# Kernel optimization log

Measured on AMD Instinct MI355X. Metric: run time of the kernel, lower is better.

Reference implementation:

```python
import jax, jax.numpy as jnp
import numpy as np

H, F = 4, 32          # num_of_heads, num_out_features
HF = H * F            # 128
F_IN = 128
EDGE_DIM = 64
HIDDEN = 256
B = 64
MLE = 1500
N = B * MLE           # 96000
E = 600000
LN_EPS = 1e-5


def setup_inputs() -> dict:
    key = jax.random.key(0)
    ks = jax.random.split(key, 20)

    def glorot(k, shape):
        fan_in, fan_out = shape[-2], shape[-1]
        lim = np.sqrt(6.0 / (fan_in + fan_out))
        return jax.random.uniform(k, shape, jnp.float32, -lim, lim)

    inp = {
        "in_nodes_features": jax.random.normal(ks[0], (N, F_IN), jnp.float32),
        "edge_index": jax.random.randint(ks[1], (2, E), 0, N),
        "edges": jax.random.normal(ks[2], (E, EDGE_DIM), jnp.float32),
        "instructions": jax.random.normal(ks[3], (B, HIDDEN), jnp.float32),
        "batch_ids": jax.random.randint(ks[4], (E,), 0, B),
        "max_local_entity": MLE,
        # parameters (stored as [in, out]; torch Linear is x @ W.T)
        "W_proj": glorot(ks[5], (F_IN, HF)),
        "W_edge": glorot(ks[6], (EDGE_DIM, HF)),
        "W_src_ins": glorot(ks[7], (HIDDEN, HF)),
        "b_src_ins": jnp.zeros((HF,), jnp.float32),
        "W_trg_ins": glorot(ks[8], (HIDDEN, HF)),
        "b_trg_ins": jnp.zeros((HF,), jnp.float32),
        "W_edge_ins": glorot(ks[9], (HIDDEN, HF)),
        "b_edge_ins": jnp.zeros((HF,), jnp.float32),
        "a_src": glorot(ks[10], (1, H, F)),
        "a_trg": glorot(ks[11], (1, H, F)),
        "a_edge": glorot(ks[12], (1, H, F)),
        "bias": jnp.zeros((HF,), jnp.float32),
        "W_skip": glorot(ks[13], (F_IN, HF)),
        "ln_gamma": jnp.ones((2 * HF,), jnp.float32),
        "ln_beta": jnp.zeros((2 * HF,), jnp.float32),
    }
    return inp


def _segment_softmax(scores, seg_idx, num_nodes):
    # scores: [E, H]; softmax over edges sharing the same seg_idx node
    s = scores - jax.lax.stop_gradient(scores.max())  # global-max shift, as in original
    e = jnp.exp(s)
    denom = jax.ops.segment_sum(e, seg_idx, num_segments=num_nodes)  # [N, H]
    return (e / (denom[seg_idx] + 1e-16))[..., None]  # [E, H, 1]


def _branch(proj, lift_idx, agg_idx, scores_per_edge, x, W_skip, bias, num_nodes):
    att = _segment_softmax(scores_per_edge, agg_idx, num_nodes)          # [E,H,1]
    weighted = proj[lift_idx] * att                                      # [E,H,F]
    out = jax.ops.segment_sum(weighted, agg_idx, num_segments=num_nodes) # [N,H,F]
    out = out + (x @ W_skip).reshape(num_nodes, H, F)                    # skip (F != F_in path)
    out = out.reshape(num_nodes, HF) + bias                              # concat heads + bias
    return out


def reference(in_nodes_features, edge_index, edges, instructions, batch_ids,
              max_local_entity, W_proj, W_edge, W_src_ins, b_src_ins,
              W_trg_ins, b_trg_ins, W_edge_ins, b_edge_ins,
              a_src, a_trg, a_edge, bias, W_skip, ln_gamma, ln_beta):
    x = in_nodes_features                      # dropout disabled (eval / p=0)
    num_nodes = x.shape[0]
    b = instructions.shape[0]
    src_idx, trg_idx = edge_index[0], edge_index[1]

    proj = (x @ W_proj).reshape(num_nodes, H, F)           # [N,H,F]
    eproj = (edges @ W_edge).reshape(-1, H, F)             # [E,H,F]

    def bridge(Wi, bi):  # instruction -> per-node [N,H,F]
        br = instructions @ Wi + bi                        # [B,HF]
        br = jnp.broadcast_to(br[:, None, :], (b, max_local_entity, HF))
        return br.reshape(num_nodes, H, F)

    src_br = bridge(W_src_ins, b_src_ins)
    trg_br = bridge(W_trg_ins, b_trg_ins)
    edge_br = (instructions @ W_edge_ins + b_edge_ins)[batch_ids].reshape(-1, H, F)

    scores_source = (proj * a_src * src_br).sum(-1)        # [N,H]
    scores_target = (proj * a_trg * trg_br).sum(-1)        # [N,H]
    scores_edge = (eproj * a_edge * edge_br).sum(-1)       # [E,H]

    scores_per_edge = jax.nn.leaky_relu(
        scores_source[src_idx] + scores_target[trg_idx] + scores_edge,
        negative_slope=0.2)                                # [E,H]

    # direction == 'all': aggregate src->trg and trg->src
    trg_feats = _branch(proj, src_idx, trg_idx, scores_per_edge, x, W_skip, bias, num_nodes)
    src_feats = _branch(proj, trg_idx, src_idx, scores_per_edge, x, W_skip, bias, num_nodes)

    out = jnp.concatenate([src_feats, trg_feats], axis=1)  # [N, 2*HF]
    mu = out.mean(-1, keepdims=True)
    var = ((out - mu) ** 2).mean(-1, keepdims=True)
    return (out - mu) * jax.lax.rsqrt(var + LN_EPS) * ln_gamma + ln_beta
```

## Files before the change

kernel.cpp:

```cpp
#include <hip/hip_runtime.h>
#include <stdint.h>

typedef unsigned short ushortT;
typedef __attribute__((ext_vector_type(8))) short short8;
typedef __attribute__((ext_vector_type(4))) float float4_;

#define HH 4
#define FF 32
#define HFD 128
#define F_IN 128
#define EDGE_DIM 64
#define HIDDEN 256
#define BB 64
#define MLE 1500
#define NN 96000
#define EEc 600000
#define CAP 32

__device__ __forceinline__ float bf_lo(uint32_t u){ return __uint_as_float(u << 16); }
__device__ __forceinline__ float bf_hi(uint32_t u){ return __uint_as_float(u & 0xffff0000u); }
__device__ __forceinline__ uint32_t f2bf(float f){
    uint32_t u = __float_as_uint(f);
    return (u + 0x7fffu + ((u >> 16) & 1u)) >> 16;
}
__device__ __forceinline__ short8 cvt8(const float* p){
    float4_ x0 = *(const float4_*)p;
    float4_ x1 = *(const float4_*)(p + 4);
    short8 r;
    r[0]=(short)f2bf(x0[0]); r[1]=(short)f2bf(x0[1]); r[2]=(short)f2bf(x0[2]); r[3]=(short)f2bf(x0[3]);
    r[4]=(short)f2bf(x1[0]); r[5]=(short)f2bf(x1[1]); r[6]=(short)f2bf(x1[2]); r[7]=(short)f2bf(x1[3]);
    return r;
}

__global__ void k_bridge(const float* ins, const float* Wsrc, const float* bsrc,
                         const float* Wtrg, const float* btrg,
                         const float* Wedg, const float* bedg,
                         const float* a_src, const float* a_trg, const float* a_edge,
                         const float* W_edge,
                         float* csrc, float* ctrg, float* Mout)
{
    __shared__ float ins_s[HIDDEN];
    __shared__ float ce_s[HFD];
    int b = blockIdx.x, t = threadIdx.x;
    const float* ip = ins + b * HIDDEN;
    ins_s[t]       = ip[t];
    ins_s[t + 128] = ip[t + 128];
    __syncthreads();
    float as = 0.f, at = 0.f, ae = 0.f;
    for (int k = 0; k < HIDDEN; k++){
        float iv = ins_s[k];
        as += iv * Wsrc[k*HFD + t];
        at += iv * Wtrg[k*HFD + t];
        ae += iv * Wedg[k*HFD + t];
    }
    csrc[b*HFD + t] = (as + bsrc[t]) * a_src[t];
    ctrg[b*HFD + t] = (at + btrg[t]) * a_trg[t];
    ce_s[t] = (ae + bedg[t]) * a_edge[t];
    __syncthreads();
    #pragma unroll
    for (int rep = 0; rep < 2; rep++){
        int idx = t + rep * 128;
        int d = idx >> 2, h = idx & 3;
        float acc = 0.f;
        #pragma unroll
        for (int f = 0; f < FF; f++)
            acc += W_edge[d*HFD + h*FF + f] * ce_s[h*FF + f];
        Mout[b*256 + d*4 + h] = acc;
    }
}

__global__ void k_transpose(const float* Wp, const float* Wsk, ushortT* WcatT)
{
    int idx = blockIdx.x * 256 + threadIdx.x;
    int c = idx >> 7;
    int d = idx & 127;
    float v = (c < 128) ? Wp[d*128 + c] : Wsk[d*128 + (c - 128)];
    WcatT[c*128 + d] = (ushortT)f2bf(v);
}

__global__ __launch_bounds__(256) void k_gemm(const float* x, const ushortT* WcatT,
                                              const float* csrc, const float* ctrg,
                                              ushortT* proj, ushortT* skip,
                                              float* s_src, float* s_trg)
{
    int t = threadIdx.x;
    int w = t >> 6, lane = t & 63;
    int q = lane >> 4, n16 = lane & 15;
    size_t node = (size_t)blockIdx.x * 64 + w * 16 + n16;

    float4_ acc[16];
    #pragma unroll
    for (int j = 0; j < 16; j++) acc[j] = (float4_){0.f, 0.f, 0.f, 0.f};

    #pragma unroll
    for (int kk = 0; kk < 4; kk++){
        short8 bfrag = cvt8(x + node * 128 + kk*32 + q*8);
        #pragma unroll
        for (int j = 0; j < 16; j++){
            short8 afrag = *(const short8*)(WcatT + (size_t)(j*16 + n16) * 128 + kk*32 + q*8);
            acc[j] = __builtin_amdgcn_mfma_f32_16x16x32_bf16(afrag, bfrag, acc[j], 0, 0, 0);
        }
    }

    #pragma unroll
    for (int j = 0; j < 16; j++){
        uint32_t p0 = f2bf(acc[j][0]) | (f2bf(acc[j][1]) << 16);
        uint32_t p1 = f2bf(acc[j][2]) | (f2bf(acc[j][3]) << 16);
        ushortT* base = (j < 8) ? (proj + node*128 + j*16 + q*4)
                                : (skip + node*128 + (j-8)*16 + q*4);
        uint2 pv; pv.x = p0; pv.y = p1;
        *(uint2*)base = pv;
    }

    int b = (int)(node / MLE);
    const float* cs = csrc + b * HFD;
    const float* ct = ctrg + b * HFD;
    float ps[4] = {0,0,0,0}, pt[4] = {0,0,0,0};
    #pragma unroll
    for (int j = 0; j < 8; j++){
        int h = j >> 1;
        #pragma unroll
        for (int r = 0; r < 4; r++){
            int c = j*16 + q*4 + r;
            ps[h] += acc[j][r] * cs[c];
            pt[h] += acc[j][r] * ct[c];
        }
    }
    #pragma unroll
    for (int m = 16; m < 64; m <<= 1){
        #pragma unroll
        for (int hh = 0; hh < 4; hh++){
            ps[hh] += __shfl_xor(ps[hh], m, 64);
            pt[hh] += __shfl_xor(pt[hh], m, 64);
        }
    }
    float vs = (q == 0) ? ps[0] : (q == 1) ? ps[1] : (q == 2) ? ps[2] : ps[3];
    float vt = (q == 0) ? pt[0] : (q == 1) ? pt[1] : (q == 2) ? pt[2] : pt[3];
    s_src[node*4 + q] = vs;
    s_trg[node*4 + q] = vt;
}

__global__ __launch_bounds__(256) void k_edges(const int* eidx, const int* bids,
    const float* edges, const float* M, const float* s_src, const float* s_trg,
    float* ex, int* cnt_src, int* cnt_trg, uint32_t* adj_src, uint32_t* adj_trg)
{
    int e = blockIdx.x * 256 + threadIdx.x;
    if (e >= EEc) return;
    int src = eidx[e];
    int trg = eidx[EEc + e];
    int bid = bids[e];
    const float* Mb = M + bid * 256;
    const float4_* er = (const float4_*)(edges + (size_t)e * EDGE_DIM);
    float se0=0.f, se1=0.f, se2=0.f, se3=0.f;
    #pragma unroll
    for (int i = 0; i < 16; i++){
        float4_ v = er[i];
        #pragma unroll
        for (int c = 0; c < 4; c++){
            int d = i*4 + c;
            float4_ m = *(const float4_*)(Mb + d*4);
            se0 += v[c]*m[0];
            se1 += v[c]*m[1];
            se2 += v[c]*m[2];
            se3 += v[c]*m[3];
        }
    }
    float4_ ssv = *(const float4_*)(s_src + (size_t)src*4);
    float4_ stv = *(const float4_*)(s_trg + (size_t)trg*4);
    float sc0 = ssv[0] + stv[0] + se0;
    float sc1 = ssv[1] + stv[1] + se1;
    float sc2 = ssv[2] + stv[2] + se2;
    float sc3 = ssv[3] + stv[3] + se3;
    sc0 = sc0 > 0.f ? sc0 : 0.2f*sc0;
    sc1 = sc1 > 0.f ? sc1 : 0.2f*sc1;
    sc2 = sc2 > 0.f ? sc2 : 0.2f*sc2;
    sc3 = sc3 > 0.f ? sc3 : 0.2f*sc3;
    float4_ exv = {__expf(sc0), __expf(sc1), __expf(sc2), __expf(sc3)};
    *(float4_*)(ex + (size_t)e*4) = exv;

    int sl = atomicAdd(&cnt_src[src], 1);
    if (sl < CAP) adj_src[(size_t)src*CAP + sl] = (uint32_t)e;
    int sl2 = atomicAdd(&cnt_trg[trg], 1);
    if (sl2 < CAP) adj_trg[(size_t)trg*CAP + sl2] = (uint32_t)e;
}

__global__ __launch_bounds__(256) void k_agg(const ushortT* proj, const ushortT* skip,
    const float* bias, const float* ex, const int* eidx,
    const int* cnt_src, const int* cnt_trg,
    const uint32_t* adj_src, const uint32_t* adj_trg,
    const float* gamma, const float* beta, float* out)
{
    __shared__ int   sh_nbr[2][4][CAP];
    __shared__ float sh_ev [2][4][CAP*4];

    int wave = threadIdx.x >> 6, lane = threadIdx.x & 63;
    int n = blockIdx.x * 4 + wave;
    int h = lane >> 4;

    int cnt0 = cnt_src[n]; if (cnt0 > CAP) cnt0 = CAP;
    int cnt1 = cnt_trg[n]; if (cnt1 > CAP) cnt1 = CAP;

    if (lane < cnt0){
        int e = (int)adj_src[(size_t)n * CAP + lane];
        sh_nbr[0][wave][lane] = eidx[EEc + e];
        *(float4_*)&sh_ev[0][wave][lane*4] = *(const float4_*)(ex + (size_t)e*4);
    }
    if (lane < cnt1){
        int e = (int)adj_trg[(size_t)n * CAP + lane];
        sh_nbr[1][wave][lane] = eidx[e];
        *(float4_*)&sh_ev[1][wave][lane*4] = *(const float4_*)(ex + (size_t)e*4);
    }

    uint32_t sv = ((const uint32_t*)(skip + (size_t)n * 128))[lane];
    float b0 = bias[2*lane], b1 = bias[2*lane + 1];

    __syncthreads();

    float sk0 = bf_lo(sv) + b0;
    float sk1 = bf_hi(sv) + b1;

    float a0 = 0.f, a1 = 0.f, ad = 0.f;
    #pragma unroll 4
    for (int i = 0; i < cnt0; i++){
        int nbr  = sh_nbr[0][wave][i];
        float ev = sh_ev[0][wave][i*4 + h];
        uint32_t pv = ((const uint32_t*)(proj + (size_t)nbr * 128))[lane];
        a0 += ev * bf_lo(pv);
        a1 += ev * bf_hi(pv);
        ad += ev;
    }
    float inv = 1.f / (ad + 1e-16f);
    float f0 = a0 * inv + sk0;
    float f1 = a1 * inv + sk1;

    a0 = 0.f; a1 = 0.f; ad = 0.f;
    #pragma unroll 4
    for (int i = 0; i < cnt1; i++){
        int nbr  = sh_nbr[1][wave][i];
        float ev = sh_ev[1][wave][i*4 + h];
        uint32_t pv = ((const uint32_t*)(proj + (size_t)nbr * 128))[lane];
        a0 += ev * bf_lo(pv);
        a1 += ev * bf_hi(pv);
        ad += ev;
    }
    inv = 1.f / (ad + 1e-16f);
    float f2 = a0 * inv + sk0;
    float f3 = a1 * inv + sk1;

    float s  = f0 + f1 + f2 + f3;
    float sq = f0*f0 + f1*f1 + f2*f2 + f3*f3;
    #pragma unroll
    for (int m = 1; m < 64; m <<= 1){
        s  += __shfl_xor(s,  m, 64);
        sq += __shfl_xor(sq, m, 64);
    }
    float mu  = s * (1.f/256.f);
    float var = sq * (1.f/256.f) - mu*mu;
    var = var < 0.f ? 0.f : var;
    float rr = rsqrtf(var + 1e-5f);

    float o0 = (f0 - mu) * rr * gamma[2*lane]           + beta[2*lane];
    float o1 = (f1 - mu) * rr * gamma[2*lane + 1]       + beta[2*lane + 1];
    float o2 = (f2 - mu) * rr * gamma[128 + 2*lane]     + beta[128 + 2*lane];
    float o3 = (f3 - mu) * rr * gamma[128 + 2*lane + 1] + beta[128 + 2*lane + 1];

    float* orow = out + (size_t)n * 256;
    *(float2*)(orow + 2*lane)       = make_float2(o0, o1);
    *(float2*)(orow + 128 + 2*lane) = make_float2(o2, o3);
}

extern "C" void kernel_launch(void* const* d_in, const int* in_sizes, int n_in,
                              void* d_out, int out_size, void* d_ws, size_t ws_size,
                              hipStream_t stream)
{
    const float* x      = (const float*)d_in[0];
    const int*   eidx   = (const int*)d_in[1];
    const float* edges  = (const float*)d_in[2];
    const float* ins    = (const float*)d_in[3];
    const int*   bids   = (const int*)d_in[4];
    const float* Wproj  = (const float*)d_in[6];
    const float* Wedge  = (const float*)d_in[7];
    const float* Wsrc   = (const float*)d_in[8];
    const float* bsrc   = (const float*)d_in[9];
    const float* Wtrg   = (const float*)d_in[10];
    const float* btrg   = (const float*)d_in[11];
    const float* Wedgi  = (const float*)d_in[12];
    const float* bedgi  = (const float*)d_in[13];
    const float* a_src  = (const float*)d_in[14];
    const float* a_trg  = (const float*)d_in[15];
    const float* a_edge = (const float*)d_in[16];
    const float* bias   = (const float*)d_in[17];
    const float* Wskip  = (const float*)d_in[18];
    const float* gamma  = (const float*)d_in[19];
    const float* beta   = (const float*)d_in[20];

    char* ws = (char*)d_ws;
    size_t off = 0;
    ushortT* proj  = (ushortT*)(ws + off); off += (size_t)NN * 128 * 2;
    ushortT* skip  = (ushortT*)(ws + off); off += (size_t)NN * 128 * 2;
    ushortT* WcatT = (ushortT*)(ws + off); off += 256 * 128 * 2;
    float*   csrc  = (float*)(ws + off);   off += BB * HFD * 4;
    float*   ctrg  = (float*)(ws + off);   off += BB * HFD * 4;
    float*   M     = (float*)(ws + off);   off += BB * 256 * 4;
    float*   s_src = (float*)(ws + off);   off += (size_t)NN * 4 * 4;
    float*   s_trg = (float*)(ws + off);   off += (size_t)NN * 4 * 4;
    float*   ex    = (float*)(ws + off);   off += (size_t)EEc * 4 * 4;
    int*     cnt_src = (int*)(ws + off);   off += (size_t)NN * 4;
    int*     cnt_trg = (int*)(ws + off);   off += (size_t)NN * 4;
    uint32_t* adj_src = (uint32_t*)(ws + off); off += (size_t)NN * CAP * 4;
    uint32_t* adj_trg = (uint32_t*)(ws + off); off += (size_t)NN * CAP * 4;

    hipMemsetAsync(cnt_src, 0, (size_t)NN * 4 * 2, stream);

    k_bridge<<<dim3(BB), dim3(128), 0, stream>>>(ins, Wsrc, bsrc, Wtrg, btrg, Wedgi, bedgi,
                                                 a_src, a_trg, a_edge, Wedge, csrc, ctrg, M);
    k_transpose<<<dim3(128), dim3(256), 0, stream>>>(Wproj, Wskip, WcatT);
    k_gemm<<<dim3(NN/64), dim3(256), 0, stream>>>(x, WcatT, csrc, ctrg, proj, skip, s_src, s_trg);
    k_edges<<<dim3((EEc + 255)/256), dim3(256), 0, stream>>>(eidx, bids, edges, M, s_src, s_trg,
                                                             ex, cnt_src, cnt_trg, adj_src, adj_trg);
    k_agg<<<dim3(NN/4), dim3(256), 0, stream>>>(proj, skip, bias, ex, eidx, cnt_src, cnt_trg,
                                                adj_src, adj_trg, gamma, beta, (float*)d_out);
}
```

Before: 603.8 us.

## Coalesce edge-feature reads in k_edges using 16 lanes per edge

k_edges is restructured so that 16 lanes share each edge row. Each lane loads one float4 of the 64-dim edge feature, so global reads are coalesced instead of each thread streaming its own 256-byte row. To match, the bridge matrix M is stored head-major, partial dot products are reduced with cross-lane shuffles, and each lane then writes one head's exp score. Only one lane per edge does the adjacency atomics. The cost is extra shuffle work and redundant src/trg index loads per lane.

Result: faster. 556.7 us (-7.8%).

```diff
diff --git a/kernel.cpp b/kernel.cpp
--- a/kernel.cpp
+++ b/kernel.cpp
@@ -65,7 +65,7 @@
         #pragma unroll
         for (int f = 0; f < FF; f++)
             acc += W_edge[d*HFD + h*FF + f] * ce_s[h*FF + f];
-        Mout[b*256 + d*4 + h] = acc;
+        Mout[b*256 + h*64 + d] = acc;
     }
 }
 
@@ -144,44 +144,75 @@
     const float* edges, const float* M, const float* s_src, const float* s_trg,
     float* ex, int* cnt_src, int* cnt_trg, uint32_t* adj_src, uint32_t* adj_trg)
 {
-    int e = blockIdx.x * 256 + threadIdx.x;
-    if (e >= EEc) return;
+    int t = threadIdx.x;
+    int wave = t >> 6, l = t & 63;
+    int g = l >> 4, s = l & 15;
+    int eb = (blockIdx.x * 4 + wave) * 16;
+
+    float4_ ev[4];
+    int bidv[4];
+    #pragma unroll
+    for (int i = 0; i < 4; i++){
+        int r = i*4 + g;
+        ev[i]   = *(const float4_*)(edges + (size_t)(eb + r) * 64 + s*4);
+        bidv[i] = bids[eb + r];
+    }
+
+    float p00=0.f,p01=0.f,p02=0.f,p03=0.f;
+    float p10=0.f,p11=0.f,p12=0.f,p13=0.f;
+    float p20=0.f,p21=0.f,p22=0.f,p23=0.f;
+    float p30=0.f,p31=0.f,p32=0.f,p33=0.f;
+    #pragma unroll
+    for (int i = 0; i < 4; i++){
+        const float* Mb = M + (size_t)bidv[i] * 256;
+        float4_ m0 = *(const float4_*)(Mb +   0 + s*4);
+        float4_ m1 = *(const float4_*)(Mb +  64 + s*4);
+        float4_ m2 = *(const float4_*)(Mb + 128 + s*4);
+        float4_ m3 = *(const float4_*)(Mb + 192 + s*4);
+        float4_ e4 = ev[i];
+        float d0 = e4[0]*m0[0] + e4[1]*m0[1] + e4[2]*m0[2] + e4[3]*m0[3];
+        float d1 = e4[0]*m1[0] + e4[1]*m1[1] + e4[2]*m1[2] + e4[3]*m1[3];
+        float d2 = e4[0]*m2[0] + e4[1]*m2[1] + e4[2]*m2[2] + e4[3]*m2[3];
+        float d3 = e4[0]*m3[0] + e4[1]*m3[1] + e4[2]*m3[2] + e4[3]*m3[3];
+        if (i == 0){ p00=d0; p01=d1; p02=d2; p03=d3; }
+        if (i == 1){ p10=d0; p11=d1; p12=d2; p13=d3; }
+        if (i == 2){ p20=d0; p21=d1; p22=d2; p23=d3; }
+        if (i == 3){ p30=d0; p31=d1; p32=d2; p33=d3; }
+    }
+
+    #pragma unroll
+    for (int mm = 1; mm < 16; mm <<= 1){
+        p00 += __shfl_xor(p00, mm, 64); p01 += __shfl_xor(p01, mm, 64);
+        p02 += __shfl_xor(p02, mm, 64); p03 += __shfl_xor(p03, mm, 64);
+        p10 += __shfl_xor(p10, mm, 64); p11 += __shfl_xor(p11, mm, 64);
+        p12 += __shfl_xor(p12, mm, 64); p13 += __shfl_xor(p13, mm, 64);
+        p20 += __shfl_xor(p20, mm, 64); p21 += __shfl_xor(p21, mm, 64);
+        p22 += __shfl_xor(p22, mm, 64); p23 += __shfl_xor(p23, mm, 64);
+        p30 += __shfl_xor(p30, mm, 64); p31 += __shfl_xor(p31, mm, 64);
+        p32 += __shfl_xor(p32, mm, 64); p33 += __shfl_xor(p33, mm, 64);
+    }
+
+    int i_sel = s >> 2;
+    int h_sel = s & 3;
+    float q0 = h_sel==0 ? p00 : h_sel==1 ? p01 : h_sel==2 ? p02 : p03;
+    float q1 = h_sel==0 ? p10 : h_sel==1 ? p11 : h_sel==2 ? p12 : p13;
+    float q2 = h_sel==0 ? p20 : h_sel==1 ? p21 : h_sel==2 ? p22 : p23;
+    float q3 = h_sel==0 ? p30 : h_sel==1 ? p31 : h_sel==2 ? p32 : p33;
+    float se = i_sel==0 ? q0 : i_sel==1 ? q1 : i_sel==2 ? q2 : q3;
+
+    int e   = eb + i_sel*4 + g;
     int src = eidx[e];
     int trg = eidx[EEc + e];
-    int bid = bids[e];
-    const float* Mb = M + bid * 256;
-    const float4_* er = (const float4_*)(edges + (size_t)e * EDGE_DIM);
-    float se0=0.f, se1=0.f, se2=0.f, se3=0.f;
-    #pragma unroll
-    for (int i = 0; i < 16; i++){
-        float4_ v = er[i];
-        #pragma unroll
-        for (int c = 0; c < 4; c++){
-            int d = i*4 + c;
-            float4_ m = *(const float4_*)(Mb + d*4);
-            se0 += v[c]*m[0];
-            se1 += v[c]*m[1];
-            se2 += v[c]*m[2];
-            se3 += v[c]*m[3];
-        }
-    }
-    float4_ ssv = *(const float4_*)(s_src + (size_t)src*4);
-    float4_ stv = *(const float4_*)(s_trg + (size_t)trg*4);
-    float sc0 = ssv[0] + stv[0] + se0;
-    float sc1 = ssv[1] + stv[1] + se1;
-    float sc2 = ssv[2] + stv[2] + se2;
-    float sc3 = ssv[3] + stv[3] + se3;
-    sc0 = sc0 > 0.f ? sc0 : 0.2f*sc0;
-    sc1 = sc1 > 0.f ? sc1 : 0.2f*sc1;
-    sc2 = sc2 > 0.f ? sc2 : 0.2f*sc2;
-    sc3 = sc3 > 0.f ? sc3 : 0.2f*sc3;
-    float4_ exv = {__expf(sc0), __expf(sc1), __expf(sc2), __expf(sc3)};
-    *(float4_*)(ex + (size_t)e*4) = exv;
-
-    int sl = atomicAdd(&cnt_src[src], 1);
-    if (sl < CAP) adj_src[(size_t)src*CAP + sl] = (uint32_t)e;
-    int sl2 = atomicAdd(&cnt_trg[trg], 1);
-    if (sl2 < CAP) adj_trg[(size_t)trg*CAP + sl2] = (uint32_t)e;
+    float sc = s_src[(size_t)src*4 + h_sel] + s_trg[(size_t)trg*4 + h_sel] + se;
+    sc = sc > 0.f ? sc : 0.2f * sc;
+    ex[(size_t)e*4 + h_sel] = __expf(sc);
+
+    if (h_sel == 0){
+        int sl = atomicAdd(&cnt_src[src], 1);
+        if (sl < CAP) adj_src[(size_t)src*CAP + sl] = (uint32_t)e;
+        int sl2 = atomicAdd(&cnt_trg[trg], 1);
+        if (sl2 < CAP) adj_trg[(size_t)trg*CAP + sl2] = (uint32_t)e;
+    }
 }
 
 __global__ __launch_bounds__(256) void k_agg(const ushortT* proj, const ushortT* skip,
@@ -247,14 +278,14 @@
     float f2 = a0 * inv + sk0;
     float f3 = a1 * inv + sk1;
 
-    float s  = f0 + f1 + f2 + f3;
+    float sum  = f0 + f1 + f2 + f3;
     float sq = f0*f0 + f1*f1 + f2*f2 + f3*f3;
     #pragma unroll
     for (int m = 1; m < 64; m <<= 1){
-        s  += __shfl_xor(s,  m, 64);
-        sq += __shfl_xor(sq, m, 64);
-    }
-    float mu  = s * (1.f/256.f);
+        sum += __shfl_xor(sum, m, 64);
+        sq  += __shfl_xor(sq,  m, 64);
+    }
+    float mu  = sum * (1.f/256.f);
     float var = sq * (1.f/256.f) - mu*mu;
     var = var < 0.f ? 0.f : var;
     float rr = rsqrtf(var + 1e-5f);
@@ -316,8 +347,8 @@
                                                  a_src, a_trg, a_edge, Wedge, csrc, ctrg, M);
     k_transpose<<<dim3(128), dim3(256), 0, stream>>>(Wproj, Wskip, WcatT);
     k_gemm<<<dim3(NN/64), dim3(256), 0, stream>>>(x, WcatT, csrc, ctrg, proj, skip, s_src, s_trg);
-    k_edges<<<dim3((EEc + 255)/256), dim3(256), 0, stream>>>(eidx, bids, edges, M, s_src, s_trg,
-                                                             ex, cnt_src, cnt_trg, adj_src, adj_trg);
+    k_edges<<<dim3(EEc/64), dim3(256), 0, stream>>>(eidx, bids, edges, M, s_src, s_trg,
+                                                    ex, cnt_src, cnt_trg, adj_src, adj_trg);
     k_agg<<<dim3(NN/4), dim3(256), 0, stream>>>(proj, skip, bias, ex, eidx, cnt_src, cnt_trg,
                                                 adj_src, adj_trg, gamma, beta, (float*)d_out);
 }
```
